# Kernel tuning notes

Measured on AMD Instinct MI355X. Metric: run time of the kernel, lower is better.

The kernel has to match this reference:

```python
import jax, jax.numpy as jnp
import numpy as np

H = 128   # hidden_dim
E = 768   # embedding_dim
L = 20    # num_layers
B = 64    # batch
T = 512   # seq_len


def setup_inputs() -> dict:
    key = jax.random.key(0)
    ks = jax.random.split(key, 9)
    k = 1.0 / np.sqrt(H)  # PyTorch LSTM default init scale
    u = lambda kk, shape: jax.random.uniform(kk, shape, jnp.float32, -k, k)
    return {
        "x": jax.random.normal(ks[0], (B, T, E), jnp.float32),
        "Wih0": u(ks[1], (4 * H, E)),        # layer 0 input weights
        "Whh0": u(ks[2], (4 * H, H)),
        "bih0": u(ks[3], (4 * H,)),
        "bhh0": u(ks[4], (4 * H,)),
        "Wih": u(ks[5], (L - 1, 4 * H, H)),  # layers 1..19
        "Whh": u(ks[6], (L - 1, 4 * H, H)),
        "bih": u(ks[7], (L - 1, 4 * H)),
        "bhh": u(ks[8], (L - 1, 4 * H)),
    }


def _lstm_layer(xs, Wih, Whh, b):
    # xs: [T, B, Din] -> ys: [T, B, H], h_final: [B, H]
    bsz = xs.shape[1]
    pre = jnp.einsum('tbd,gd->tbg', xs, Wih) + b  # precompute input projections

    def step(carry, pt):
        h, c = carry
        g = pt + h @ Whh.T  # [B, 4H]
        i, f, gg, o = jnp.split(g, 4, axis=-1)  # PyTorch gate order i,f,g,o
        i = jax.nn.sigmoid(i)
        f = jax.nn.sigmoid(f)
        gg = jnp.tanh(gg)
        o = jax.nn.sigmoid(o)
        c = f * c + i * gg
        h = o * jnp.tanh(c)
        return (h, c), h

    init = (jnp.zeros((bsz, H), xs.dtype), jnp.zeros((bsz, H), xs.dtype))
    (_, _), ys = jax.lax.scan(step, init, pre)
    return ys, ys[-1]


def reference(x, Wih0, Whh0, bih0, bhh0, Wih, Whh, bih, bhh):
    xs = jnp.swapaxes(x, 0, 1)  # [T, B, E]
    ys, _ = _lstm_layer(xs, Wih0, Whh0, bih0 + bhh0)

    def layer_fn(ys, params):
        Wl, Wh, bi, bh = params
        ys2, h = _lstm_layer(ys, Wl, Wh, bi + bh)
        return ys2, h

    ys, hs = jax.lax.scan(layer_fn, ys, (Wih, Whh, bih, bhh))
    return hs[-1]  # hidden state of last (20th) layer at final timestep: [B, H]
```

## Files before the change

### kernel.cpp

```cpp
#include <hip/hip_runtime.h>

#define H4 128
#define EE 768
#define NL 20
#define BB 64
#define TT 512
#define G4 512
#define NBG 8
#define CK 16
#define NCH (TT/CK)
#define RC 2

typedef _Float16 v8h __attribute__((ext_vector_type(8)));
typedef _Float16 v4h __attribute__((ext_vector_type(4)));
typedef float v4f __attribute__((ext_vector_type(4)));
typedef unsigned int v4u __attribute__((ext_vector_type(4)));

#if defined(__has_builtin)
#if __has_builtin(__builtin_amdgcn_exp2f) && __has_builtin(__builtin_amdgcn_rcpf)
#define EXP2F __builtin_amdgcn_exp2f
#define RCPF  __builtin_amdgcn_rcpf
#endif
#endif
#ifndef EXP2F
#define EXP2F exp2f
#define RCPF(x) (1.0f/(x))
#endif

__device__ __forceinline__ float fast_sig(float x) {
  float e = EXP2F(-1.44269504f * x);
  return RCPF(1.0f + e);
}
__device__ __forceinline__ float fast_tanh(float x) {
  float e = EXP2F(2.88539008f * x);
  return 1.0f - 2.0f * RCPF(1.0f + e);
}

__device__ __forceinline__ int swz(int row, int byteInRow) {
  return (row * 256 + byteInRow) ^ ((row & 7) << 4);
}

__global__ __launch_bounds__(256) void prep_kernel(
    const float* __restrict__ Wih0, const float* __restrict__ Whh0,
    const float* __restrict__ bih,  const float* __restrict__ bhh,
    const float* __restrict__ Wih,  const float* __restrict__ Whh,
    _Float16* __restrict__ W0h, _Float16* __restrict__ Wc,
    float* __restrict__ biasc, unsigned* __restrict__ flags)
{
  long idx = (long)blockIdx.x * 256 + threadIdx.x;
  const long NWC = (long)NL * G4 * 256;
  const long NW0 = (long)G4 * EE;
  const long NBI = (long)NL * G4;
  if (idx < NWC) {
    int l = (int)(idx >> 17);
    int rem = (int)(idx & 131071);
    int n = rem >> 8, kk = rem & 255;
    float v;
    if (l == 0) v = (kk < 128) ? 0.0f : Whh0[n * H4 + kk - 128];
    else v = (kk < 128) ? Wih[((long)(l-1) * G4 + n) * H4 + kk]
                        : Whh[((long)(l-1) * G4 + n) * H4 + kk - 128];
    Wc[idx] = (_Float16)v;
  } else if ((idx -= NWC) < NW0) {
    W0h[idx] = (_Float16)Wih0[idx];
  } else if ((idx -= NW0) < NBI) {
    int l = (int)(idx >> 9), n = (int)(idx & 511);
    biasc[idx] = (l == 0) ? 0.0f : (bih[(l-1) * G4 + n] + bhh[(l-1) * G4 + n]);
  } else if ((idx -= NBI) < 256) {
    flags[idx] = 0u;
  }
}

__global__ __launch_bounds__(512) void pre0_gemm(
    const float* __restrict__ x, const _Float16* __restrict__ W0h,
    const float* __restrict__ bih0, const float* __restrict__ bhh0,
    _Float16* __restrict__ pre0)
{
  __shared__ __align__(16) unsigned char smem[46080];
  _Float16* sA = (_Float16*)smem;
  _Float16* sB = (_Float16*)(smem + 5120);
  _Float16* sC = (_Float16*)smem;
  int t = blockIdx.x;
  int tid = threadIdx.x;
  int w = tid >> 6, lane = tid & 63;
  int l15 = lane & 15, kb = lane >> 4;

  v4f acc[4][4];
#pragma unroll
  for (int mi = 0; mi < 4; ++mi)
#pragma unroll
    for (int ni = 0; ni < 4; ++ni) acc[mi][ni] = (v4f){0.f, 0.f, 0.f, 0.f};

  int bA = tid >> 3, kqA = tid & 7;
  const float* xp = x + ((long)bA * TT + t) * EE + kqA * 4;
  const _Float16* wp = W0h + (long)tid * EE;

  for (int k0 = 0; k0 < EE; k0 += 32) {
    float4 xv = *(const float4*)(xp + k0);
    v4h xh = { (_Float16)xv.x, (_Float16)xv.y, (_Float16)xv.z, (_Float16)xv.w };
    *(v4h*)&sA[bA * 40 + kqA * 4] = xh;
#pragma unroll
    for (int c = 0; c < 4; ++c)
      *(v8h*)&sB[tid * 40 + c * 8] = *(const v8h*)(wp + k0 + c * 8);
    __syncthreads();
#pragma unroll
    for (int mi = 0; mi < 4; ++mi) {
      v8h a = *(const v8h*)&sA[(16 * mi + l15) * 40 + kb * 8];
#pragma unroll
      for (int ni = 0; ni < 4; ++ni) {
        v8h b = *(const v8h*)&sB[(64 * w + 16 * ni + l15) * 40 + kb * 8];
        acc[mi][ni] = __builtin_amdgcn_mfma_f32_16x16x32_f16(a, b, acc[mi][ni], 0, 0, 0);
      }
    }
    __syncthreads();
  }

#pragma unroll
  for (int hh2 = 0; hh2 < 2; ++hh2) {
    __syncthreads();
    if ((w >> 2) == hh2) {
      int wl = w & 3;
#pragma unroll
      for (int ni = 0; ni < 4; ++ni) {
        int nloc = 64 * wl + 16 * ni + l15;
        int n = 256 * hh2 + nloc;
        float bia = bih0[n] + bhh0[n];
#pragma unroll
        for (int mi = 0; mi < 4; ++mi)
#pragma unroll
          for (int r = 0; r < 4; ++r)
            sC[nloc * 72 + 16 * mi + 4 * kb + r] = (_Float16)(acc[mi][ni][r] + bia);
      }
    }
    __syncthreads();
    int row = tid >> 1, part = tid & 1;
    _Float16* po = pre0 + ((long)t * G4 + 256 * hh2 + row) * 64 + part * 32;
#pragma unroll
    for (int c = 0; c < 4; ++c)
      *(v8h*)(po + c * 8) = *(const v8h*)&sC[row * 72 + part * 32 + c * 8];
  }
}

__global__ __launch_bounds__(512, 1) void lstm_pipe(
    const _Float16* __restrict__ pre0, const _Float16* __restrict__ Wc,
    const float* __restrict__ biasc, _Float16* __restrict__ yring,
    unsigned* __restrict__ flags, float* __restrict__ out)
{
  __shared__ __align__(16) unsigned char lds[40960];
  const int l = blockIdx.x >> 3, bg = blockIdx.x & 7;
  const int tid = threadIdx.x, w = tid >> 6, lane = tid & 63;
  const int l15 = lane & 15, kb = lane >> 4;
  const int jloc = 16 * w + l15;
  const bool valid = (kb < 2);
  const int b0 = 4 * (kb & 1);

  v8h bw[4][8];
  const _Float16* wbase = Wc + (long)l * G4 * 256;
#pragma unroll
  for (int q = 0; q < 4; ++q)
#pragma unroll
    for (int ks = 0; ks < 8; ++ks)
      bw[q][ks] = *(const v8h*)(wbase + (long)(128 * q + jloc) * 256 + ks * 32 + kb * 8);
#pragma unroll
  for (int q = 0; q < 4; ++q)
#pragma unroll
    for (int ks = 0; ks < 8; ++ks)
      asm volatile("" : "+v"(bw[q][ks]));

  float bias_q[4];
#pragma unroll
  for (int q = 0; q < 4; ++q)
    bias_q[q] = (l == 0) ? 0.0f : biasc[l * G4 + 128 * q + jloc];

  *(v4u*)(lds + 32768 + tid * 16) = (v4u){0u, 0u, 0u, 0u};

  const int myf = l * 8 + bg;
  const unsigned* fin  = flags + ((l > 0) ? (myf - 8) : myf);
  const unsigned* fout = flags + ((l < NL - 1) ? (myf + 8) : myf);
  unsigned* fme = flags + myf;
  char* ywr = (char*)(yring + (long)myf * (RC * CK * 1024));
  const char* yrd = (const char*)(yring + (long)(myf - 8) * (RC * CK * 1024));

  v4f cst = (v4f){0.f, 0.f, 0.f, 0.f};
  v4h pc[4];
  if (l == 0) {
    const _Float16* pb = pre0 + bg * 8 + b0;
#pragma unroll
    for (int q = 0; q < 4; ++q)
      pc[q] = *(const v4h*)(pb + (long)(128 * q + jloc) * 64);
  }

  __syncthreads();

  for (int c = 0; c < NCH; ++c) {
    if (l > 0) {
      unsigned f;
      for (;;) {
        asm volatile("global_load_dword %0, %1, off sc0 sc1\n\ts_waitcnt vmcnt(0)"
                     : "=v"(f) : "v"(fin));
        if (f > (unsigned)c) break;
        __builtin_amdgcn_s_sleep(2);
      }
      const char* src = yrd + (long)(c & (RC - 1)) * 32768 + tid * 16;
      v4u d0, d1, d2, d3;
      asm volatile("global_load_dwordx4 %0, %1, off sc0 sc1" : "=v"(d0) : "v"(src));
      asm volatile("global_load_dwordx4 %0, %1, off sc0 sc1" : "=v"(d1) : "v"(src + 8192));
      asm volatile("global_load_dwordx4 %0, %1, off sc0 sc1" : "=v"(d2) : "v"(src + 16384));
      asm volatile("global_load_dwordx4 %0, %1, off sc0 sc1" : "=v"(d3) : "v"(src + 24576));
      asm volatile("s_waitcnt vmcnt(0)" ::: "memory");
      __builtin_amdgcn_sched_barrier(0);
      unsigned char* dst = lds + tid * 16;
      *(v4u*)(dst)         = d0;
      *(v4u*)(dst +  8192) = d1;
      *(v4u*)(dst + 16384) = d2;
      *(v4u*)(dst + 24576) = d3;
    }
    if (l < NL - 1 && c >= RC) {
      unsigned f;
      for (;;) {
        asm volatile("global_load_dword %0, %1, off sc0 sc1\n\ts_waitcnt vmcnt(0)"
                     : "=v"(f) : "v"(fout));
        if (f >= (unsigned)(c - 1)) break;
        __builtin_amdgcn_s_sleep(2);
      }
    }
    __syncthreads();

    for (int ts = 0; ts < CK; ++ts) {
      const int t = c * CK + ts;
      const int p = t & 1;
      v4f acc[4];
#pragma unroll
      for (int q = 0; q < 4; ++q)
        acc[q] = (v4f){bias_q[q], bias_q[q], bias_q[q], bias_q[q]};

      v4h pn[4];
      if (l == 0) {
#pragma unroll
        for (int q = 0; q < 4; ++q)
#pragma unroll
          for (int r = 0; r < 4; ++r) acc[q][r] += (float)pc[q][r];
        const int tn = (t + 1) & (TT - 1);
        const _Float16* pb = pre0 + (long)tn * G4 * 64 + bg * 8 + b0;
#pragma unroll
        for (int q = 0; q < 4; ++q)
          pn[q] = *(const v4h*)(pb + (long)(128 * q + jloc) * 64);
      }

      const unsigned char* hb = lds + 32768 + p * 4096;
      if (l > 0) {
        const unsigned char* yb = lds + ts * 2048;
#pragma unroll
        for (int ks = 0; ks < 4; ++ks) {
          v8h a = *(const v8h*)(yb + swz(l15, ks * 64 + kb * 16));
#pragma unroll
          for (int q = 0; q < 4; ++q)
            acc[q] = __builtin_amdgcn_mfma_f32_16x16x32_f16(a, bw[q][ks], acc[q], 0, 0, 0);
        }
      }
#pragma unroll
      for (int ks = 4; ks < 8; ++ks) {
        v8h a = *(const v8h*)(hb + swz(l15, (ks - 4) * 64 + kb * 16));
#pragma unroll
        for (int q = 0; q < 4; ++q)
          acc[q] = __builtin_amdgcn_mfma_f32_16x16x32_f16(a, bw[q][ks], acc[q], 0, 0, 0);
      }

      _Float16 hh[4]; float hf[4];
#pragma unroll
      for (int r = 0; r < 4; ++r) {
        float i_ = fast_sig(acc[0][r]);
        float f_ = fast_sig(acc[1][r]);
        float g_ = fast_tanh(acc[2][r]);
        float o_ = fast_sig(acc[3][r]);
        float cn = f_ * cst[r] + i_ * g_;
        cst[r] = cn;
        float h_ = o_ * fast_tanh(cn);
        hf[r] = h_; hh[r] = (_Float16)h_;
      }

      if (valid) {
        unsigned char* hn = lds + 32768 + (p ^ 1) * 4096;
#pragma unroll
        for (int r = 0; r < 4; ++r)
          *(_Float16*)(hn + swz(b0 + r, jloc * 2)) = hh[r];
        if (l < NL - 1) {
          char* dstb = ywr + (long)(c & (RC - 1)) * 32768 + ts * 2048;
#pragma unroll
          for (int r = 0; r < 4; ++r) {
            union { _Float16 h; unsigned short u; } cv; cv.h = hh[r];
            unsigned val = cv.u;
            char* dst = dstb + swz(b0 + r, jloc * 2);
            asm volatile("global_store_short %0, %1, off sc0 sc1"
                         :: "v"(dst), "v"(val) : "memory");
          }
        } else if (t == TT - 1) {
#pragma unroll
          for (int r = 0; r < 4; ++r)
            out[(bg * 8 + b0 + r) * H4 + jloc] = hf[r];
        }
      }
      if (l == 0) {
#pragma unroll
        for (int q = 0; q < 4; ++q) pc[q] = pn[q];
      }
      __syncthreads();
    }

    asm volatile("s_waitcnt vmcnt(0)" ::: "memory");
    __syncthreads();
    if (tid == 0) {
      unsigned v = (unsigned)(c + 1);
      asm volatile("global_store_dword %0, %1, off sc0 sc1" :: "v"(fme), "v"(v) : "memory");
    }
  }
}

extern "C" void kernel_launch(void* const* d_in, const int* in_sizes, int n_in,
                              void* d_out, int out_size, void* d_ws, size_t ws_size,
                              hipStream_t stream)
{
  const float* x    = (const float*)d_in[0];
  const float* Wih0 = (const float*)d_in[1];
  const float* Whh0 = (const float*)d_in[2];
  const float* bih0 = (const float*)d_in[3];
  const float* bhh0 = (const float*)d_in[4];
  const float* Wih  = (const float*)d_in[5];
  const float* Whh  = (const float*)d_in[6];
  const float* bih  = (const float*)d_in[7];
  const float* bhh  = (const float*)d_in[8];
  float* out = (float*)d_out;
  char* ws = (char*)d_ws;

  _Float16* pre0  = (_Float16*)(ws);
  _Float16* W0h   = (_Float16*)(ws + 33554432);
  _Float16* Wc    = (_Float16*)(ws + 34340864);
  float*    bc    = (float*)   (ws + 39583744);
  _Float16* yring = (_Float16*)(ws + 39624704);
  unsigned* flags = (unsigned*)(ws + 50110464);

  prep_kernel<<<11817, 256, 0, stream>>>(Wih0, Whh0, bih, bhh, Wih, Whh, W0h, Wc, bc, flags);
  pre0_gemm<<<TT, 512, 0, stream>>>(x, W0h, bih0, bhh0, pre0);
  lstm_pipe<<<NL * NBG, 512, 0, stream>>>(pre0, Wc, bc, yring, flags, out);
}
```

Baseline: 1.181 ms.

## Relayout layer-0 projections and coalesce inter-layer h stores via LDS

The layer-0 precomputed input projections get a new layout, [t][batch-group][gate][8 batches], so each block's per-step reads are contiguous. The layer-to-layer h handoff now writes one dword per thread, copied from the LDS h buffer after the barrier, in place of four scattered 2-byte stores per valid lane. The empty asm register pins on the weight fragments are also dropped, which gives the compiler more freedom over register allocation. Scattered global traffic on the serial recurrence should shrink, though the ring store now sits after the barrier and the weights might be rematerialized or spilled.

```diff
diff --git a/kernel.cpp b/kernel.cpp
--- a/kernel.cpp
+++ b/kernel.cpp
@@ -133,10 +133,13 @@
     }
     __syncthreads();
     int row = tid >> 1, part = tid & 1;
-    _Float16* po = pre0 + ((long)t * G4 + 256 * hh2 + row) * 64 + part * 32;
-#pragma unroll
-    for (int c = 0; c < 4; ++c)
-      *(v8h*)(po + c * 8) = *(const v8h*)&sC[row * 72 + part * 32 + c * 8];
+    int n = 256 * hh2 + row;
+#pragma unroll
+    for (int g = 0; g < 4; ++g) {
+      int bg = part * 4 + g;
+      _Float16* po = pre0 + (((long)t * 8 + bg) * 512 + n) * 8;
+      *(v8h*)po = *(const v8h*)&sC[row * 72 + part * 32 + g * 8];
+    }
   }
 }
 
@@ -160,11 +163,6 @@
 #pragma unroll
     for (int ks = 0; ks < 8; ++ks)
       bw[q][ks] = *(const v8h*)(wbase + (long)(128 * q + jloc) * 256 + ks * 32 + kb * 8);
-#pragma unroll
-  for (int q = 0; q < 4; ++q)
-#pragma unroll
-    for (int ks = 0; ks < 8; ++ks)
-      asm volatile("" : "+v"(bw[q][ks]));
 
   float bias_q[4];
 #pragma unroll
@@ -182,11 +180,11 @@
 
   v4f cst = (v4f){0.f, 0.f, 0.f, 0.f};
   v4h pc[4];
+  const _Float16* pbase0 = pre0 + (long)bg * 4096 + jloc * 8 + b0;
   if (l == 0) {
-    const _Float16* pb = pre0 + bg * 8 + b0;
 #pragma unroll
     for (int q = 0; q < 4; ++q)
-      pc[q] = *(const v4h*)(pb + (long)(128 * q + jloc) * 64);
+      pc[q] = *(const v4h*)(pbase0 + q * 1024);
   }
 
   __syncthreads();
@@ -240,10 +238,10 @@
 #pragma unroll
           for (int r = 0; r < 4; ++r) acc[q][r] += (float)pc[q][r];
         const int tn = (t + 1) & (TT - 1);
-        const _Float16* pb = pre0 + (long)tn * G4 * 64 + bg * 8 + b0;
+        const _Float16* pb = pbase0 + (long)tn * 32768;
 #pragma unroll
         for (int q = 0; q < 4; ++q)
-          pn[q] = *(const v4h*)(pb + (long)(128 * q + jloc) * 64);
+          pn[q] = *(const v4h*)(pb + q * 1024);
       }
 
       const unsigned char* hb = lds + 32768 + p * 4096;
@@ -283,17 +281,7 @@
 #pragma unroll
         for (int r = 0; r < 4; ++r)
           *(_Float16*)(hn + swz(b0 + r, jloc * 2)) = hh[r];
-        if (l < NL - 1) {
-          char* dstb = ywr + (long)(c & (RC - 1)) * 32768 + ts * 2048;
-#pragma unroll
-          for (int r = 0; r < 4; ++r) {
-            union { _Float16 h; unsigned short u; } cv; cv.h = hh[r];
-            unsigned val = cv.u;
-            char* dst = dstb + swz(b0 + r, jloc * 2);
-            asm volatile("global_store_short %0, %1, off sc0 sc1"
-                         :: "v"(dst), "v"(val) : "memory");
-          }
-        } else if (t == TT - 1) {
+        if (l == NL - 1 && t == TT - 1) {
 #pragma unroll
           for (int r = 0; r < 4; ++r)
             out[(bg * 8 + b0 + r) * H4 + jloc] = hf[r];
@@ -304,6 +292,13 @@
         for (int q = 0; q < 4; ++q) pc[q] = pn[q];
       }
       __syncthreads();
+
+      if (l < NL - 1) {
+        unsigned hv = *(const unsigned*)(lds + 32768 + (p ^ 1) * 4096 + tid * 4);
+        char* dst = ywr + (long)(c & (RC - 1)) * 32768 + ts * 2048 + tid * 4;
+        asm volatile("global_store_dword %0, %1, off sc0 sc1"
+                     :: "v"(dst), "v"(hv) : "memory");
+      }
     }
 
     asm volatile("s_waitcnt vmcnt(0)" ::: "memory");
```

Result: faster. 1.101 ms (-6.7%).
